# Optimization experiments

Hardware: AMD Instinct MI355X
Metric: run time of the kernel (lower is better)

## Reference

```python
import jax, jax.numpy as jnp
import numpy as np

NUM_EMBEDDINGS = 4096
EMBEDDING_DIM = 64
COMMITMENT_COST = 0.25
DECAY = 0.99
EPSILON = 1e-05


def setup_inputs() -> dict:
    key = jax.random.key(0)
    k1, k2, k3, k4 = jax.random.split(key, 4)
    z = jax.random.normal(k1, (128, 24, 1536), dtype=jnp.float32)
    embedding = jax.random.normal(k2, (NUM_EMBEDDINGS, EMBEDDING_DIM), dtype=jnp.float32) * 0.05
    ema_cluster_size = jax.random.uniform(k3, (NUM_EMBEDDINGS,), dtype=jnp.float32)
    ema_w = jax.random.normal(k4, (NUM_EMBEDDINGS, EMBEDDING_DIM), dtype=jnp.float32) * 0.05
    return {"z": z, "embedding": embedding, "ema_cluster_size": ema_cluster_size, "ema_w": ema_w}


def reference(z, embedding, ema_cluster_size, ema_w):
    # VectorQuantizer.forward in training mode (EMA codebook update).
    K, d = embedding.shape
    B = z.shape[0]
    z_flat = z.reshape(-1, d)  # [N, d], N = B*576

    # Pairwise squared distances: ||z||^2 + ||e||^2 - 2 z e^T  -> [N, K]
    dist = (jnp.sum(z_flat * z_flat, axis=1, keepdims=True)
            + jnp.sum(embedding * embedding, axis=1)
            - 2.0 * (z_flat @ embedding.T))
    codes = jnp.argmin(dist, axis=1)  # [N]

    # EMA statistics (one-hot scatter expressed as segment sums)
    counts = jax.ops.segment_sum(jnp.ones_like(codes, dtype=z.dtype), codes, num_segments=K)
    new_cluster_size = DECAY * ema_cluster_size + (1.0 - DECAY) * counts
    dw = jax.ops.segment_sum(z_flat, codes, num_segments=K)  # [K, d]
    new_ema_w = DECAY * ema_w + (1.0 - DECAY) * dw

    n = jnp.sum(new_cluster_size)
    cluster_size = (new_cluster_size + EPSILON) / (n + K * EPSILON) * n
    new_embedding = new_ema_w / cluster_size[:, None]

    # Quantize with the UPDATED codebook (torch copies weights before embedding lookup)
    z_q = new_embedding[codes].reshape(z.shape)
    vq_loss = COMMITMENT_COST * jnp.mean((jax.lax.stop_gradient(z_q) - z) ** 2)
    z_q_st = z + jax.lax.stop_gradient(z_q - z)  # straight-through
    codes = codes.reshape(B, -1)  # [B, 576]
    return (vq_loss, z_q_st, codes, new_embedding, new_cluster_size, new_ema_w)
```

## Files before the change

kernel.cpp:

```cpp
#include <hip/hip_runtime.h>

constexpr int KC    = 4096;
constexpr int DIM   = 64;
constexpr int NROWS = 73728;
constexpr int NELEM = 4718592;
constexpr int GSTRIDE = 4160;

typedef _Float16 f16x8 __attribute__((ext_vector_type(8)));
typedef float    f32x4 __attribute__((ext_vector_type(4)));

constexpr size_t OUT_LOSS  = 0;
constexpr size_t OUT_ZQ    = 1;
constexpr size_t OUT_CODES = 1 + (size_t)NELEM;
constexpr size_t OUT_EMB   = OUT_CODES + (size_t)NROWS;
constexpr size_t OUT_NCS   = OUT_EMB + (size_t)KC * DIM;
constexpr size_t OUT_NEW   = OUT_NCS + (size_t)KC;

constexpr size_t alignup(size_t x, size_t a) { return (x + a - 1) & ~(a - 1); }
constexpr size_t WS_CODES  = 0;
constexpr size_t WS_COUNTS = WS_CODES + sizeof(int) * (size_t)NROWS;
constexpr size_t WS_OFFS   = WS_COUNTS + sizeof(int) * (size_t)KC;
constexpr size_t WS_CURSOR = alignup(WS_OFFS + sizeof(int) * (KC + 1), 16);
constexpr size_t WS_SORTED = WS_CURSOR + sizeof(int) * (size_t)KC;
constexpr size_t WS_N      = alignup(WS_SORTED + sizeof(int) * (size_t)NROWS, 16);
constexpr size_t WS_LOSSD  = alignup(WS_N + sizeof(float), 8);
constexpr size_t WS_EMBPK  = alignup(WS_LOSSD + 8, 64);

__global__ void k_prep(const float* __restrict__ emb, char* __restrict__ emb_pk,
                       int* __restrict__ counts) {
    if (threadIdx.x < 32) counts[blockIdx.x * 32 + threadIdx.x] = 0;
    int t = blockIdx.x * 256 + threadIdx.x;
    int c = t >> 3, q = t & 7;
    const float* ep = emb + (size_t)c * DIM + q * 8;
    f16x8 hv, lv;
    float s = 0.f;
    #pragma unroll
    for (int e = 0; e < 8; ++e) {
        float x = ep[e];
        _Float16 h = (_Float16)x;
        float r = x - (float)h;
        hv[e] = h;
        lv[e] = (_Float16)(r * 2048.0f);
        s = fmaf(x, x, s);
    }
    s += __shfl_xor(s, 1, 64);
    s += __shfl_xor(s, 2, 64);
    s += __shfl_xor(s, 4, 64);
    int g = c >> 4, lc = c & 15;
    int h = q >> 2, lq = q & 3;
    int lane = lq * 16 + lc;
    char* gbase = emb_pk + (size_t)g * GSTRIDE;
    if (q == 0) *(float*)(gbase + lc * 4) = 1024.0f * s;
    char* base = gbase + 64 + lane * 16;
    *(f16x8*)(base + h * 1024)       = hv;
    *(f16x8*)(base + (2 + h) * 1024) = lv;
}

__global__ __launch_bounds__(192, 2) void k_argmin7(
        const float* __restrict__ z, const char* __restrict__ emb_pk,
        int* __restrict__ codes_i, float* __restrict__ codes_f,
        int* __restrict__ counts) {
    __shared__ int codebuf[3][48];

    const int tid = threadIdx.x;
    const int l   = tid & 63;
    const int w   = tid >> 6;
    const int lc  = l & 15;
    const int lq  = l >> 4;
    const int waveRow = blockIdx.x * 144 + w * 48;

    f16x8 ah2k[3][2], ahr[3][2], al2k[3][2];
    #pragma unroll
    for (int rt = 0; rt < 3; ++rt)
        #pragma unroll
        for (int h = 0; h < 2; ++h) {
            const float* zp = z + (size_t)(waveRow + rt * 16 + lc) * DIM + h * 32 + lq * 8;
            float4 x0 = *(const float4*)zp;
            float4 x1 = *(const float4*)(zp + 4);
            float xs[8] = {x0.x, x0.y, x0.z, x0.w, x1.x, x1.y, x1.z, x1.w};
            #pragma unroll
            for (int e = 0; e < 8; ++e) {
                _Float16 hh = (_Float16)xs[e];
                float rr = xs[e] - (float)hh;
                ahr[rt][h][e]  = -hh;
                ah2k[rt][h][e] = (_Float16)(-2048.0f * (float)hh);
                al2k[rt][h][e] = -(_Float16)(rr * 2048.0f);
            }
        }

    float best[3][4];
    int   bestg[3][4];
    #pragma unroll
    for (int rt = 0; rt < 3; ++rt)
        #pragma unroll
        for (int j = 0; j < 4; ++j) { best[rt][j] = INFINITY; bestg[rt][j] = 0; }

    const unsigned long long pkb = (unsigned long long)emb_pk;
    unsigned voffA = 64 + l * 16;
    unsigned voffB = lc * 4;

    f16x8 b00, b01, b02, b03, b10, b11, b12, b13;
    f16x8 b20, b21, b22, b23, b30, b31, b32, b33;
    float e0, e1, e2v, e3;

#define ISSUE(B0, B1, B2, B3, EV)                                                        \
    asm volatile("global_load_dword %0, %1, %2"             : "=v"(EV) : "v"(voffB), "s"(pkb)); \
    asm volatile("global_load_dwordx4 %0, %1, %2"             : "=v"(B0) : "v"(voffA), "s"(pkb)); \
    asm volatile("global_load_dwordx4 %0, %1, %2 offset:1024" : "=v"(B1) : "v"(voffA), "s"(pkb)); \
    asm volatile("global_load_dwordx4 %0, %1, %2 offset:2048" : "=v"(B2) : "v"(voffA), "s"(pkb)); \
    asm volatile("global_load_dwordx4 %0, %1, %2 offset:3072" : "=v"(B3) : "v"(voffA), "s"(pkb)); \
    voffA += GSTRIDE; voffB += GSTRIDE;

#define WAITP                                                \
    asm volatile("s_waitcnt vmcnt(15)" ::: "memory");        \
    __builtin_amdgcn_sched_barrier(0);

#define COMP(B0, B1, B2, B3, EV, G) {                                             \
        f32x4 ci; ci[0] = EV; ci[1] = EV; ci[2] = EV; ci[3] = EV;                 \
        _Pragma("unroll")                                                         \
        for (int rt = 0; rt < 3; ++rt) {                                          \
            f32x4 acc = __builtin_amdgcn_mfma_f32_16x16x32_f16(ah2k[rt][0], B0, ci, 0, 0, 0); \
            acc = __builtin_amdgcn_mfma_f32_16x16x32_f16(ah2k[rt][1], B1, acc, 0, 0, 0);      \
            acc = __builtin_amdgcn_mfma_f32_16x16x32_f16(ahr[rt][0],  B2, acc, 0, 0, 0);      \
            acc = __builtin_amdgcn_mfma_f32_16x16x32_f16(ahr[rt][1],  B3, acc, 0, 0, 0);      \
            acc = __builtin_amdgcn_mfma_f32_16x16x32_f16(al2k[rt][0], B0, acc, 0, 0, 0);      \
            acc = __builtin_amdgcn_mfma_f32_16x16x32_f16(al2k[rt][1], B1, acc, 0, 0, 0);      \
            _Pragma("unroll")                                                     \
            for (int j = 0; j < 4; ++j) {                                         \
                if (acc[j] < best[rt][j]) { best[rt][j] = acc[j]; bestg[rt][j] = (G); } \
            }                                                                     \
        } }

    __builtin_amdgcn_sched_barrier(0);
    ISSUE(b00, b01, b02, b03, e0)
    ISSUE(b10, b11, b12, b13, e1)
    ISSUE(b20, b21, b22, b23, e2v)
    ISSUE(b30, b31, b32, b33, e3)

    for (int g = 0; g < 256; g += 4) {
        WAITP  COMP(b00, b01, b02, b03, e0,  g)      ISSUE(b00, b01, b02, b03, e0)
        WAITP  COMP(b10, b11, b12, b13, e1,  g + 1)  ISSUE(b10, b11, b12, b13, e1)
        WAITP  COMP(b20, b21, b22, b23, e2v, g + 2)  ISSUE(b20, b21, b22, b23, e2v)
        WAITP  COMP(b30, b31, b32, b33, e3,  g + 3)  ISSUE(b30, b31, b32, b33, e3)
    }
    asm volatile("s_waitcnt vmcnt(0)" ::: "memory");
    __builtin_amdgcn_sched_barrier(0);
#undef ISSUE
#undef WAITP
#undef COMP

    #pragma unroll
    for (int rt = 0; rt < 3; ++rt)
        #pragma unroll
        for (int j = 0; j < 4; ++j) {
            float b = best[rt][j];
            int   k = bestg[rt][j] * 16 + lc;
            #pragma unroll
            for (int m = 1; m < 16; m <<= 1) {
                float obv = __shfl_xor(b, m, 64);
                int   okv = __shfl_xor(k, m, 64);
                if (obv < b || (obv == b && okv < k)) { b = obv; k = okv; }
            }
            if (lc == 0) codebuf[w][rt * 16 + lq * 4 + j] = k;
        }

    if (l < 48) {
        int code = codebuf[w][l];
        size_t rowg = (size_t)waveRow + l;
        codes_i[rowg] = code;
        codes_f[rowg] = (float)code;
        atomicAdd(&counts[code], 1);
    }
}

__global__ void k_scan(const int* __restrict__ counts,
                       int* __restrict__ offsets, int* __restrict__ cursor,
                       const float* __restrict__ ema_cs, float* __restrict__ ncs_out,
                       float* __restrict__ n_out, double* __restrict__ lossp) {
    __shared__ int   part[256];
    __shared__ float fpart[256];
    int tid = threadIdx.x;
    if (tid == 0) *lossp = 0.0;
    int base = tid * 16;
    int loc[16];
    int s = 0;
    float fs = 0.f;
    #pragma unroll
    for (int j = 0; j < 16; ++j) {
        int cnt = counts[base + j];
        loc[j] = s; s += cnt;
        float v = 0.99f * ema_cs[base + j] + 0.01f * (float)cnt;
        ncs_out[base + j] = v;
        fs += v;
    }
    part[tid] = s;
    fpart[tid] = fs;
    __syncthreads();
    for (int off = 1; off < 256; off <<= 1) {
        int v = (tid >= off) ? part[tid - off] : 0;
        __syncthreads();
        part[tid] += v;
        __syncthreads();
    }
    int excl = part[tid] - s;
    #pragma unroll
    for (int j = 0; j < 16; ++j) {
        int o = excl + loc[j];
        offsets[base + j] = o;
        cursor[base + j]  = o;
    }
    if (tid == 255) offsets[KC] = excl + s;
    for (int m = 128; m > 0; m >>= 1) {
        if (tid < m) fpart[tid] += fpart[tid + m];
        __syncthreads();
    }
    if (tid == 0) n_out[0] = fpart[0];
}

__global__ void k_scatteridx(const int* __restrict__ codes_i,
                             int* __restrict__ cursor, int* __restrict__ sorted_rows) {
    int r = blockIdx.x * 256 + threadIdx.x;
    if (r < NROWS) {
        int c = codes_i[r];
        int p = atomicAdd(&cursor[c], 1);
        sorted_rows[p] = r;
    }
}

__global__ __launch_bounds__(64) void k_dwsum(
        const float* __restrict__ z, const int* __restrict__ offsets,
        const int* __restrict__ sorted_rows, const float* __restrict__ ema_w,
        const float* __restrict__ ncs, const float* __restrict__ nptr,
        float* __restrict__ new_ema_w_out, float* __restrict__ new_emb_out) {
    int k = blockIdx.x, tid = threadIdx.x;
    int beg = offsets[k], end = offsets[k + 1];
    float a0 = 0.f, a1 = 0.f, a2 = 0.f, a3 = 0.f;
    int i = beg;
    for (; i + 3 < end; i += 4) {
        int r0 = sorted_rows[i], r1 = sorted_rows[i + 1];
        int r2 = sorted_rows[i + 2], r3 = sorted_rows[i + 3];
        a0 += z[(size_t)r0 * DIM + tid];
        a1 += z[(size_t)r1 * DIM + tid];
        a2 += z[(size_t)r2 * DIM + tid];
        a3 += z[(size_t)r3 * DIM + tid];
    }
    for (; i < end; ++i) a0 += z[(size_t)sorted_rows[i] * DIM + tid];
    float dwv = (a0 + a1) + (a2 + a3);
    size_t idx = (size_t)k * DIM + tid;
    float n = nptr[0];
    float nw = 0.99f * ema_w[idx] + 0.01f * dwv;
    float cs = (ncs[k] + 1e-5f) / (n + 4096.0f * 1e-5f) * n;
    new_ema_w_out[idx] = nw;
    new_emb_out[idx] = nw / cs;
}

__global__ __launch_bounds__(256) void k_quant(
        const float* __restrict__ z, const float* __restrict__ new_emb,
        const int* __restrict__ codes, float* __restrict__ zq_out,
        double* __restrict__ loss_acc) {
    __shared__ double red[256];
    const int nvec = NELEM / 4;
    int t = blockIdx.x * 256 + threadIdx.x;
    int stride = gridDim.x * 256;
    double ls = 0.0;
    for (int v = t; v < nvec; v += stride) {
        int e0 = v * 4;
        int n  = e0 >> 6;
        int d0 = e0 & 63;
        int code = codes[n];
        float4 zq = *(const float4*)&new_emb[(size_t)code * DIM + d0];
        float4 zv = *(const float4*)&z[e0];
        float dx = zq.x - zv.x, dy = zq.y - zv.y, dz = zq.z - zv.z, dw4 = zq.w - zv.w;
        float4 o;
        o.x = zv.x + dx; o.y = zv.y + dy; o.z = zv.z + dz; o.w = zv.w + dw4;
        *(float4*)&zq_out[e0] = o;
        ls += (double)(dx * dx) + (double)(dy * dy) + (double)(dz * dz) + (double)(dw4 * dw4);
    }
    red[threadIdx.x] = ls;
    __syncthreads();
    for (int m = 128; m > 0; m >>= 1) {
        if (threadIdx.x < m) red[threadIdx.x] += red[threadIdx.x + m];
        __syncthreads();
    }
    if (threadIdx.x == 0) atomicAdd(loss_acc, red[0]);
}

__global__ void k_loss(const double* __restrict__ loss_acc, float* __restrict__ out0) {
    out0[0] = (float)(0.25 * (loss_acc[0] / (double)NELEM));
}

extern "C" void kernel_launch(void* const* d_in, const int* in_sizes, int n_in,
                              void* d_out, int out_size, void* d_ws, size_t ws_size,
                              hipStream_t stream) {
    const float* z      = (const float*)d_in[0];
    const float* emb    = (const float*)d_in[1];
    const float* ema_cs = (const float*)d_in[2];
    const float* ema_w  = (const float*)d_in[3];
    float* out = (float*)d_out;
    char*  ws  = (char*)d_ws;

    int*    codes_i = (int*)(ws + WS_CODES);
    int*    counts  = (int*)(ws + WS_COUNTS);
    int*    offsets = (int*)(ws + WS_OFFS);
    int*    cursor  = (int*)(ws + WS_CURSOR);
    int*    sorted  = (int*)(ws + WS_SORTED);
    float*  nptr    = (float*)(ws + WS_N);
    double* lossp   = (double*)(ws + WS_LOSSD);
    char*   emb_pk  = ws + WS_EMBPK;

    k_prep<<<(KC * 8) / 256, 256, 0, stream>>>(emb, emb_pk, counts);
    k_argmin7<<<NROWS / 144, 192, 0, stream>>>(z, emb_pk, codes_i,
                                               out + OUT_CODES, counts);
    k_scan<<<1, 256, 0, stream>>>(counts, offsets, cursor, ema_cs,
                                  out + OUT_NCS, nptr, lossp);
    k_scatteridx<<<(NROWS + 255) / 256, 256, 0, stream>>>(codes_i, cursor, sorted);
    k_dwsum<<<KC, 64, 0, stream>>>(z, offsets, sorted, ema_w,
                                   out + OUT_NCS, nptr, out + OUT_NEW, out + OUT_EMB);
    k_quant<<<1152, 256, 0, stream>>>(z, out + OUT_EMB, codes_i,
                                      out + OUT_ZQ, lossp);
    k_loss<<<1, 1, 0, stream>>>(lossp, out + OUT_LOSS);
}
```

Measured before the change: 167.6 us.

## Fuse quantize and loss into per-code dw kernel with ticket finalization

Merges the z_q/straight-through write and loss accumulation into the per-code segment-sum kernel. Each block re-walks its sorted rows, computes the new embedding row locally, writes z_q and accumulates squared error. The last block, found with an atomic ticket, writes the final loss. This removes two launches and the codes/new_emb gather pass. In exchange, z rows are read twice through a scattered index, and work per block is skewed by cluster size. The argmin loop also becomes branchless select/fminf with unroll 1, and the final prefetch is redirected to group 0 so it stays in bounds.

After: 296.1 us. 76.7% more time.

```diff
diff --git a/kernel.cpp b/kernel.cpp
--- a/kernel.cpp
+++ b/kernel.cpp
@@ -23,7 +23,8 @@
 constexpr size_t WS_CURSOR = alignup(WS_OFFS + sizeof(int) * (KC + 1), 16);
 constexpr size_t WS_SORTED = WS_CURSOR + sizeof(int) * (size_t)KC;
 constexpr size_t WS_N      = alignup(WS_SORTED + sizeof(int) * (size_t)NROWS, 16);
-constexpr size_t WS_LOSSD  = alignup(WS_N + sizeof(float), 8);
+constexpr size_t WS_TICKET = WS_N + sizeof(float);
+constexpr size_t WS_LOSSD  = alignup(WS_TICKET + sizeof(int), 8);
 constexpr size_t WS_EMBPK  = alignup(WS_LOSSD + 8, 64);
 
 __global__ void k_prep(const float* __restrict__ emb, char* __restrict__ emb_pk,
@@ -56,7 +57,7 @@
     *(f16x8*)(base + (2 + h) * 1024) = lv;
 }
 
-__global__ __launch_bounds__(192, 2) void k_argmin7(
+__global__ __launch_bounds__(192, 2) void k_argmin14(
         const float* __restrict__ z, const char* __restrict__ emb_pk,
         int* __restrict__ codes_i, float* __restrict__ codes_f,
         int* __restrict__ counts) {
@@ -96,8 +97,10 @@
         for (int j = 0; j < 4; ++j) { best[rt][j] = INFINITY; bestg[rt][j] = 0; }
 
     const unsigned long long pkb = (unsigned long long)emb_pk;
-    unsigned voffA = 64 + l * 16;
-    unsigned voffB = lc * 4;
+    const unsigned voffA0 = 64 + l * 16;
+    const unsigned voffB0 = lc * 4;
+    unsigned voffA = voffA0;
+    unsigned voffB = voffB0;
 
     f16x8 b00, b01, b02, b03, b10, b11, b12, b13;
     f16x8 b20, b21, b22, b23, b30, b31, b32, b33;
@@ -127,7 +130,8 @@
             acc = __builtin_amdgcn_mfma_f32_16x16x32_f16(al2k[rt][1], B1, acc, 0, 0, 0);      \
             _Pragma("unroll")                                                     \
             for (int j = 0; j < 4; ++j) {                                         \
-                if (acc[j] < best[rt][j]) { best[rt][j] = acc[j]; bestg[rt][j] = (G); } \
+                bestg[rt][j] = (acc[j] < best[rt][j]) ? (G) : bestg[rt][j];       \
+                best[rt][j]  = fminf(best[rt][j], acc[j]);                        \
             }                                                                     \
         } }
 
@@ -137,7 +141,9 @@
     ISSUE(b20, b21, b22, b23, e2v)
     ISSUE(b30, b31, b32, b33, e3)
 
+    #pragma unroll 1
     for (int g = 0; g < 256; g += 4) {
+        if (g == 252) { voffA = voffA0; voffB = voffB0; }
         WAITP  COMP(b00, b01, b02, b03, e0,  g)      ISSUE(b00, b01, b02, b03, e0)
         WAITP  COMP(b10, b11, b12, b13, e1,  g + 1)  ISSUE(b10, b11, b12, b13, e1)
         WAITP  COMP(b20, b21, b22, b23, e2v, g + 2)  ISSUE(b20, b21, b22, b23, e2v)
@@ -176,11 +182,12 @@
 __global__ void k_scan(const int* __restrict__ counts,
                        int* __restrict__ offsets, int* __restrict__ cursor,
                        const float* __restrict__ ema_cs, float* __restrict__ ncs_out,
-                       float* __restrict__ n_out, double* __restrict__ lossp) {
+                       float* __restrict__ n_out, double* __restrict__ lossp,
+                       int* __restrict__ ticket) {
     __shared__ int   part[256];
     __shared__ float fpart[256];
     int tid = threadIdx.x;
-    if (tid == 0) *lossp = 0.0;
+    if (tid == 0) { *lossp = 0.0; *ticket = 0; }
     int base = tid * 16;
     int loc[16];
     int s = 0;
@@ -227,11 +234,13 @@
     }
 }
 
-__global__ __launch_bounds__(64) void k_dwsum(
+__global__ __launch_bounds__(64) void k_dwtail(
         const float* __restrict__ z, const int* __restrict__ offsets,
         const int* __restrict__ sorted_rows, const float* __restrict__ ema_w,
         const float* __restrict__ ncs, const float* __restrict__ nptr,
-        float* __restrict__ new_ema_w_out, float* __restrict__ new_emb_out) {
+        float* __restrict__ new_ema_w_out, float* __restrict__ new_emb_out,
+        float* __restrict__ zq_out, double* __restrict__ loss_acc,
+        int* __restrict__ ticket, float* __restrict__ out0) {
     int k = blockIdx.x, tid = threadIdx.x;
     int beg = offsets[k], end = offsets[k + 1];
     float a0 = 0.f, a1 = 0.f, a2 = 0.f, a3 = 0.f;
@@ -250,43 +259,29 @@
     float n = nptr[0];
     float nw = 0.99f * ema_w[idx] + 0.01f * dwv;
     float cs = (ncs[k] + 1e-5f) / (n + 4096.0f * 1e-5f) * n;
+    float ne = nw / cs;
     new_ema_w_out[idx] = nw;
-    new_emb_out[idx] = nw / cs;
-}
-
-__global__ __launch_bounds__(256) void k_quant(
-        const float* __restrict__ z, const float* __restrict__ new_emb,
-        const int* __restrict__ codes, float* __restrict__ zq_out,
-        double* __restrict__ loss_acc) {
-    __shared__ double red[256];
-    const int nvec = NELEM / 4;
-    int t = blockIdx.x * 256 + threadIdx.x;
-    int stride = gridDim.x * 256;
+    new_emb_out[idx] = ne;
+
     double ls = 0.0;
-    for (int v = t; v < nvec; v += stride) {
-        int e0 = v * 4;
-        int n  = e0 >> 6;
-        int d0 = e0 & 63;
-        int code = codes[n];
-        float4 zq = *(const float4*)&new_emb[(size_t)code * DIM + d0];
-        float4 zv = *(const float4*)&z[e0];
-        float dx = zq.x - zv.x, dy = zq.y - zv.y, dz = zq.z - zv.z, dw4 = zq.w - zv.w;
-        float4 o;
-        o.x = zv.x + dx; o.y = zv.y + dy; o.z = zv.z + dz; o.w = zv.w + dw4;
-        *(float4*)&zq_out[e0] = o;
-        ls += (double)(dx * dx) + (double)(dy * dy) + (double)(dz * dz) + (double)(dw4 * dw4);
-    }
-    red[threadIdx.x] = ls;
-    __syncthreads();
-    for (int m = 128; m > 0; m >>= 1) {
-        if (threadIdx.x < m) red[threadIdx.x] += red[threadIdx.x + m];
-        __syncthreads();
-    }
-    if (threadIdx.x == 0) atomicAdd(loss_acc, red[0]);
-}
-
-__global__ void k_loss(const double* __restrict__ loss_acc, float* __restrict__ out0) {
-    out0[0] = (float)(0.25 * (loss_acc[0] / (double)NELEM));
+    for (i = beg; i < end; ++i) {
+        int r = sorted_rows[i];
+        float zv = z[(size_t)r * DIM + tid];
+        float d = ne - zv;
+        zq_out[(size_t)r * DIM + tid] = zv + d;
+        ls += (double)d * (double)d;
+    }
+    #pragma unroll
+    for (int m = 32; m > 0; m >>= 1) ls += __shfl_down(ls, m, 64);
+    if (tid == 0) {
+        if (ls != 0.0) atomicAdd(loss_acc, ls);
+        __threadfence();
+        int t = atomicAdd(ticket, 1);
+        if (t == KC - 1) {
+            double L = atomicAdd(loss_acc, 0.0);
+            out0[0] = (float)(0.25 * (L / (double)NELEM));
+        }
+    }
 }
 
 extern "C" void kernel_launch(void* const* d_in, const int* in_sizes, int n_in,
@@ -305,18 +300,17 @@
     int*    cursor  = (int*)(ws + WS_CURSOR);
     int*    sorted  = (int*)(ws + WS_SORTED);
     float*  nptr    = (float*)(ws + WS_N);
+    int*    ticket  = (int*)(ws + WS_TICKET);
     double* lossp   = (double*)(ws + WS_LOSSD);
     char*   emb_pk  = ws + WS_EMBPK;
 
     k_prep<<<(KC * 8) / 256, 256, 0, stream>>>(emb, emb_pk, counts);
-    k_argmin7<<<NROWS / 144, 192, 0, stream>>>(z, emb_pk, codes_i,
-                                               out + OUT_CODES, counts);
+    k_argmin14<<<NROWS / 144, 192, 0, stream>>>(z, emb_pk, codes_i,
+                                                out + OUT_CODES, counts);
     k_scan<<<1, 256, 0, stream>>>(counts, offsets, cursor, ema_cs,
-                                  out + OUT_NCS, nptr, lossp);
+                                  out + OUT_NCS, nptr, lossp, ticket);
     k_scatteridx<<<(NROWS + 255) / 256, 256, 0, stream>>>(codes_i, cursor, sorted);
-    k_dwsum<<<KC, 64, 0, stream>>>(z, offsets, sorted, ema_w,
-                                   out + OUT_NCS, nptr, out + OUT_NEW, out + OUT_EMB);
-    k_quant<<<1152, 256, 0, stream>>>(z, out + OUT_EMB, codes_i,
-                                      out + OUT_ZQ, lossp);
-    k_loss<<<1, 1, 0, stream>>>(lossp, out + OUT_LOSS);
-}
+    k_dwtail<<<KC, 64, 0, stream>>>(z, offsets, sorted, ema_w,
+                                    out + OUT_NCS, nptr, out + OUT_NEW, out + OUT_EMB,
+                                    out + OUT_ZQ, lossp, ticket, out + OUT_LOSS);
+}
```
